# Kernel tuning notes

Measured on AMD Instinct MI355X. Metric: run time of the kernel, lower is better.

## Reference

```python
import jax, jax.numpy as jnp
import numpy as np

# Model dims (Gemma-class)
B, T, HID = 1, 3072, 2048
H, KH, D = 16, 8, 128          # q heads, kv heads, head_dim
WIN = 1024                     # sliding window
EPS = 1e-6
SEQ = 1536                     # two packed sequences of length 1536


def _rms(x, w):
    # torch nn.RMSNorm: x * rsqrt(mean(x^2) + eps) [* weight]
    var = jnp.mean(x * x, axis=-1, keepdims=True)
    y = x * jax.lax.rsqrt(var + EPS)
    return y if w is None else y * w


def _rotate_half(x):
    x1, x2 = jnp.split(x, 2, axis=-1)
    return jnp.concatenate([-x2, x1], axis=-1)


def _rope(x, cos, sin):
    # x: [B,T,h,D]; cos/sin: [B,T,rd] -> unsqueeze head dim (matches cos.unsqueeze(2))
    c = cos[:, :, None, :]
    s = sin[:, :, None, :]
    rd = cos.shape[-1]
    xr, xp = x[..., :rd], x[..., rd:]
    xr = xr * c + _rotate_half(xr) * s
    return jnp.concatenate([xr, xp], axis=-1)


def _build_mask(cu_seqlens):
    # causal & within sliding window & same packed sequence (matches _sliding_mask)
    idx = jnp.arange(T)
    seg = jnp.searchsorted(cu_seqlens, idx, side='right') - 1
    i = idx[:, None]
    j = idx[None, :]
    return (i >= j) & ((i - j) < WIN) & (seg[:, None] == seg[None, :])


def _attn_layer(x, wq, qn, k, v, wo, cos, sin, mask):
    # x: [B,T,HID]; k,v: [T,KH,D] (possibly shared from an earlier layer)
    q = _rope(_rms((x @ wq).reshape(B, T, H, D), qn), cos, sin).reshape(T, H, D)
    rep = H // k.shape[1]
    kk = jnp.repeat(k, rep, axis=1)   # GQA: repeat_interleave over head dim
    vv = jnp.repeat(v, rep, axis=1)
    s = jnp.einsum('qhd,khd->hqk', q, kk)          # scale = 1.0 (as in source)
    s = jnp.where(mask, s, jnp.asarray(-1e30, s.dtype))
    p = jax.nn.softmax(s, axis=-1)
    o = jnp.einsum('hqk,khd->qhd', p, vv).reshape(B, T, H * D)
    return o @ wo


def setup_inputs() -> dict:
    key = jax.random.key(0)
    ks = jax.random.split(key, 10)
    hidden_states = jax.random.normal(ks[0], (B, T, HID), jnp.float32)
    # RoPE tables with per-packed-sequence position resets
    pos = jnp.concatenate([jnp.arange(SEQ), jnp.arange(SEQ)]).astype(jnp.float32)
    inv = 1.0 / (10000.0 ** (jnp.arange(0, D, 2, dtype=jnp.float32) / D))
    fr = pos[:, None] * inv[None, :]
    emb = jnp.concatenate([fr, fr], axis=-1)     # [T, D]
    cos = jnp.cos(emb)[None]                     # [1, T, D]
    sin = jnp.sin(emb)[None]
    w = lambda k, sh: 0.02 * jax.random.normal(k, sh, jnp.float32)
    return {
        'hidden_states': hidden_states,
        'cos': cos, 'sin': sin,
        'wq0': w(ks[1], (HID, H * D)), 'wk0': w(ks[2], (HID, KH * D)),
        'wv0': w(ks[3], (HID, KH * D)), 'wo0': w(ks[4], (H * D, HID)),
        'qn0': 1.0 + 0.01 * jax.random.normal(ks[5], (D,), jnp.float32),
        'kn0': 1.0 + 0.01 * jax.random.normal(ks[6], (D,), jnp.float32),
        'wq1': w(ks[7], (HID, H * D)), 'wo1': w(ks[8], (H * D, HID)),
        'qn1': 1.0 + 0.01 * jax.random.normal(ks[9], (D,), jnp.float32),
        'cu_seqlens': jnp.array([0, SEQ, T], dtype=jnp.int32),
    }


def reference(hidden_states, cos, sin, wq0, wk0, wv0, wo0, qn0, kn0, wq1, wo1, qn1, cu_seqlens):
    mask = _build_mask(cu_seqlens)
    # Layer 0: source layer -> computes and stores K/V
    k = _rope(_rms((hidden_states @ wk0).reshape(B, T, KH, D), kn0), cos, sin).reshape(T, KH, D)
    v = _rms((hidden_states @ wv0).reshape(B, T, KH, D), None).reshape(T, KH, D)
    out0 = _attn_layer(hidden_states, wq0, qn0, k, v, wo0, cos, sin, mask)
    # Layer 1: KV-shared layer -> reuses layer 0's K/V (skips k/v projections)
    out1 = _attn_layer(out0, wq1, qn1, k, v, wo1, cos, sin, mask)
    return out1
```

## Files before the change

kernel.cpp:

```cpp
#include <hip/hip_runtime.h>
#include <hip/hip_bf16.h>

#define T_TOK 3072
#define HIDDEN 2048
#define NHQ 16
#define NHKV 8
#define DH 128
#define WINDOW 1024

typedef __attribute__((ext_vector_type(4))) float f32x4;
typedef __attribute__((ext_vector_type(8))) short bf16x8;
typedef __attribute__((ext_vector_type(8))) unsigned short ushort8;
typedef __attribute__((ext_vector_type(4))) unsigned short ushort4v;

__device__ __forceinline__ unsigned short f2bf(float f) {
  union { float fv; unsigned u; } v; v.fv = f;
  unsigned r = v.u + 0x7fffu + ((v.u >> 16) & 1u);
  return (unsigned short)(r >> 16);
}
__device__ __forceinline__ float bf2f(unsigned short h) {
  union { unsigned u; float f; } v; v.u = ((unsigned)h) << 16;
  return v.f;
}
__device__ __forceinline__ void split2(float f, unsigned short& hi, unsigned short& lo) {
  hi = f2bf(f);
  lo = f2bf(f - bf2f(hi));
}

__global__ __launch_bounds__(256) void cvt_split(const float* __restrict__ x,
                                                 unsigned short* __restrict__ yh,
                                                 unsigned short* __restrict__ yl, int n) {
  int i = (blockIdx.x * 256 + threadIdx.x) * 4;
  if (i >= n) return;
  f32x4 v = *(const f32x4*)(x + i);
  ushort4v oh, ol;
#pragma unroll
  for (int j = 0; j < 4; ++j) {
    unsigned short h, l;
    split2(v[j], h, l);
    oh[j] = h; ol[j] = l;
  }
  *(ushort4v*)(yh + i) = oh;
  *(ushort4v*)(yl + i) = ol;
}

__global__ __launch_bounds__(256) void transpose_w_split(const float* __restrict__ W,
                                                         unsigned short* __restrict__ Wth,
                                                         unsigned short* __restrict__ Wtl,
                                                         int K, int N) {
  __shared__ float tile[32][33];
  int bn = blockIdx.x * 32, bk = blockIdx.y * 32;
  int tx = threadIdx.x & 31, ty = threadIdx.x >> 5;
#pragma unroll
  for (int i = 0; i < 4; ++i)
    tile[ty + i * 8][tx] = W[(size_t)(bk + ty + i * 8) * N + bn + tx];
  __syncthreads();
#pragma unroll
  for (int i = 0; i < 4; ++i) {
    unsigned short h, l;
    split2(tile[tx][ty + i * 8], h, l);
    Wth[(size_t)(bn + ty + i * 8) * K + bk + tx] = h;
    if (Wtl) Wtl[(size_t)(bn + ty + i * 8) * K + bk + tx] = l;
  }
}

__global__ __launch_bounds__(256) void transpose_u16(const unsigned short* __restrict__ src,
                                                     unsigned short* __restrict__ dst,
                                                     int R, int C) {
  __shared__ unsigned short tile[32][33];
  int bc = blockIdx.x * 32, br = blockIdx.y * 32;
  int tx = threadIdx.x & 31, ty = threadIdx.x >> 5;
#pragma unroll
  for (int i = 0; i < 4; ++i)
    tile[ty + i * 8][tx] = src[(size_t)(br + ty + i * 8) * C + bc + tx];
  __syncthreads();
#pragma unroll
  for (int i = 0; i < 4; ++i)
    dst[(size_t)(bc + ty + i * 8) * R + br + tx] = tile[tx][ty + i * 8];
}

template <int OUT>
__global__ __launch_bounds__(256) void gemm3_64(const unsigned short* __restrict__ Ah,
                                                const unsigned short* __restrict__ Al,
                                                const unsigned short* __restrict__ Bh,
                                                const unsigned short* __restrict__ Bl,
                                                float* __restrict__ Cf,
                                                unsigned short* __restrict__ Ch,
                                                unsigned short* __restrict__ Cl,
                                                int M, int N, int K) {
  __shared__ unsigned short ah_lds[64 * 32];
  __shared__ unsigned short al_lds[64 * 32];
  __shared__ unsigned short bh_lds[128 * 32];
  __shared__ unsigned short bl_lds[128 * 32];
  const int tid = threadIdx.x, lane = tid & 63, wave = tid >> 6;
  const int wr = (wave >> 1) * 32, wc = (wave & 1) * 64;
  const int g = lane >> 4, r16 = lane & 15;
  int nwg = gridDim.x * gridDim.y;
  int id = blockIdx.y * gridDim.x + blockIdx.x;
  int nid = (id & 7) * (nwg >> 3) + (id >> 3);
  const int bm = nid % gridDim.x, bn = nid / gridDim.x;
  f32x4 acc[2][4];
#pragma unroll
  for (int i = 0; i < 2; ++i)
#pragma unroll
    for (int j = 0; j < 4; ++j) acc[i][j] = (f32x4){0.f, 0.f, 0.f, 0.f};

  const unsigned short* AhB = Ah + (size_t)bm * 64 * K;
  const unsigned short* AlB = Al + (size_t)bm * 64 * K;
  const unsigned short* BhB = Bh + (size_t)bn * 128 * K;
  const unsigned short* BlB = Bl + (size_t)bn * 128 * K;

  for (int kt = 0; kt < K; kt += 32) {
    __syncthreads();
    {
      size_t goff = (size_t)(wave * 16 + (lane >> 2)) * K + kt + (lane & 3) * 8;
      int loff = wave * 512;
      __builtin_amdgcn_global_load_lds(
          (const __attribute__((address_space(1))) unsigned int*)(AhB + goff),
          (__attribute__((address_space(3))) unsigned int*)(ah_lds + loff), 16, 0, 0);
      __builtin_amdgcn_global_load_lds(
          (const __attribute__((address_space(1))) unsigned int*)(AlB + goff),
          (__attribute__((address_space(3))) unsigned int*)(al_lds + loff), 16, 0, 0);
    }
#pragma unroll
    for (int c = 0; c < 2; ++c) {
      size_t goff = (size_t)(wave * 32 + c * 16 + (lane >> 2)) * K + kt + (lane & 3) * 8;
      int loff = (wave * 2 + c) * 512;
      __builtin_amdgcn_global_load_lds(
          (const __attribute__((address_space(1))) unsigned int*)(BhB + goff),
          (__attribute__((address_space(3))) unsigned int*)(bh_lds + loff), 16, 0, 0);
      __builtin_amdgcn_global_load_lds(
          (const __attribute__((address_space(1))) unsigned int*)(BlB + goff),
          (__attribute__((address_space(3))) unsigned int*)(bl_lds + loff), 16, 0, 0);
    }
    __syncthreads();
    bf16x8 ahf[2], alf[2], bhf[4], blf[4];
#pragma unroll
    for (int i = 0; i < 2; ++i) {
      ahf[i] = *(const bf16x8*)&ah_lds[(wr + i * 16 + r16) * 32 + g * 8];
      alf[i] = *(const bf16x8*)&al_lds[(wr + i * 16 + r16) * 32 + g * 8];
    }
#pragma unroll
    for (int j = 0; j < 4; ++j) {
      bhf[j] = *(const bf16x8*)&bh_lds[(wc + j * 16 + r16) * 32 + g * 8];
      blf[j] = *(const bf16x8*)&bl_lds[(wc + j * 16 + r16) * 32 + g * 8];
    }
#pragma unroll
    for (int i = 0; i < 2; ++i)
#pragma unroll
      for (int j = 0; j < 4; ++j) {
        acc[i][j] = __builtin_amdgcn_mfma_f32_16x16x32_bf16(ahf[i], bhf[j], acc[i][j], 0, 0, 0);
        acc[i][j] = __builtin_amdgcn_mfma_f32_16x16x32_bf16(ahf[i], blf[j], acc[i][j], 0, 0, 0);
        acc[i][j] = __builtin_amdgcn_mfma_f32_16x16x32_bf16(alf[i], bhf[j], acc[i][j], 0, 0, 0);
      }
  }

#pragma unroll
  for (int i = 0; i < 2; ++i) {
    int row = bm * 64 + wr + i * 16 + g * 4;
#pragma unroll
    for (int j = 0; j < 4; ++j) {
      int col = bn * 128 + wc + j * 16 + r16;
#pragma unroll
      for (int r = 0; r < 4; ++r) {
        if (OUT == 0) {
          Cf[(size_t)(row + r) * N + col] = acc[i][j][r];
        } else {
          unsigned short h, l;
          split2(acc[i][j][r], h, l);
          Ch[(size_t)(row + r) * N + col] = h;
          Cl[(size_t)(row + r) * N + col] = l;
        }
      }
    }
  }
}

__global__ __launch_bounds__(256) void gemm1_64(const unsigned short* __restrict__ Ah,
                                                const unsigned short* __restrict__ Bh,
                                                float* __restrict__ Cf,
                                                int M, int N, int K) {
  __shared__ unsigned short ah_lds[64 * 32];
  __shared__ unsigned short bh_lds[128 * 32];
  const int tid = threadIdx.x, lane = tid & 63, wave = tid >> 6;
  const int wr = (wave >> 1) * 32, wc = (wave & 1) * 64;
  const int g = lane >> 4, r16 = lane & 15;
  int nwg = gridDim.x * gridDim.y;
  int id = blockIdx.y * gridDim.x + blockIdx.x;
  int nid = (id & 7) * (nwg >> 3) + (id >> 3);
  const int bm = nid % gridDim.x, bn = nid / gridDim.x;
  f32x4 acc[2][4];
#pragma unroll
  for (int i = 0; i < 2; ++i)
#pragma unroll
    for (int j = 0; j < 4; ++j) acc[i][j] = (f32x4){0.f, 0.f, 0.f, 0.f};

  const unsigned short* AhB = Ah + (size_t)bm * 64 * K;
  const unsigned short* BhB = Bh + (size_t)bn * 128 * K;

  for (int kt = 0; kt < K; kt += 32) {
    __syncthreads();
    {
      size_t goff = (size_t)(wave * 16 + (lane >> 2)) * K + kt + (lane & 3) * 8;
      __builtin_amdgcn_global_load_lds(
          (const __attribute__((address_space(1))) unsigned int*)(AhB + goff),
          (__attribute__((address_space(3))) unsigned int*)(ah_lds + wave * 512), 16, 0, 0);
    }
#pragma unroll
    for (int c = 0; c < 2; ++c) {
      size_t goff = (size_t)(wave * 32 + c * 16 + (lane >> 2)) * K + kt + (lane & 3) * 8;
      __builtin_amdgcn_global_load_lds(
          (const __attribute__((address_space(1))) unsigned int*)(BhB + goff),
          (__attribute__((address_space(3))) unsigned int*)(bh_lds + (wave * 2 + c) * 512), 16, 0, 0);
    }
    __syncthreads();
    bf16x8 ahf[2], bhf[4];
#pragma unroll
    for (int i = 0; i < 2; ++i)
      ahf[i] = *(const bf16x8*)&ah_lds[(wr + i * 16 + r16) * 32 + g * 8];
#pragma unroll
    for (int j = 0; j < 4; ++j)
      bhf[j] = *(const bf16x8*)&bh_lds[(wc + j * 16 + r16) * 32 + g * 8];
#pragma unroll
    for (int i = 0; i < 2; ++i)
#pragma unroll
      for (int j = 0; j < 4; ++j)
        acc[i][j] = __builtin_amdgcn_mfma_f32_16x16x32_bf16(ahf[i], bhf[j], acc[i][j], 0, 0, 0);
  }

#pragma unroll
  for (int i = 0; i < 2; ++i) {
    int row = bm * 64 + wr + i * 16 + g * 4;
#pragma unroll
    for (int j = 0; j < 4; ++j) {
      int col = bn * 128 + wc + j * 16 + r16;
#pragma unroll
      for (int r = 0; r < 4; ++r)
        Cf[(size_t)(row + r) * N + col] = acc[i][j][r];
    }
  }
}

__global__ __launch_bounds__(256) void rms_rope_split(const float* __restrict__ X,
                                                      const float* __restrict__ w,
                                                      const float* __restrict__ cosp,
                                                      const float* __restrict__ sinp,
                                                      unsigned short* __restrict__ outh,
                                                      unsigned short* __restrict__ outl,
                                                      int NH, int doRope, int XS, int XO) {
  int row = blockIdx.x * 4 + (threadIdx.x >> 6);
  int lane = threadIdx.x & 63;
  int t = row / NH, hh_ = row % NH;
  const float* x = X + (size_t)t * XS + XO + (size_t)hh_ * DH;
  float x1 = x[lane], x2 = x[lane + 64];
  float ss = x1 * x1 + x2 * x2;
#pragma unroll
  for (int m = 1; m < 64; m <<= 1) ss += __shfl_xor(ss, m, 64);
  float inv = rsqrtf(ss * (1.0f / 128.0f) + 1e-6f);
  float y1 = x1 * inv, y2 = x2 * inv;
  if (w) { y1 *= w[lane]; y2 *= w[lane + 64]; }
  if (doRope) {
    float c1 = cosp[t * DH + lane], s1 = sinp[t * DH + lane];
    float c2 = cosp[t * DH + lane + 64], s2 = sinp[t * DH + lane + 64];
    float o1 = y1 * c1 - y2 * s1;
    float o2 = y2 * c2 + y1 * s2;
    y1 = o1; y2 = o2;
  }
  unsigned short h, l;
  split2(y1, h, l);
  outh[(size_t)row * DH + lane] = h;
  if (outl) outl[(size_t)row * DH + lane] = l;
  split2(y2, h, l);
  outh[(size_t)row * DH + lane + 64] = h;
  if (outl) outl[(size_t)row * DH + lane + 64] = l;
}

template <int WRITE_LO>
__global__ __launch_bounds__(256) void attn3(const unsigned short* __restrict__ Qh,
                                             const unsigned short* __restrict__ Ql,
                                             const unsigned short* __restrict__ Kh,
                                             const unsigned short* __restrict__ Kl,
                                             const unsigned short* __restrict__ Vth,
                                             unsigned short* __restrict__ Oh,
                                             unsigned short* __restrict__ Ol,
                                             const int* __restrict__ cu, int ncu) {
  __shared__ unsigned short kh_lds[32][136];
  __shared__ unsigned short kl_lds[32][136];
  __shared__ unsigned short vh_lds[144][40];
  __shared__ unsigned short ph_lds[4][16][44];

  int id = blockIdx.y * gridDim.x + blockIdx.x;
  int nid = (id & 7) * 96 + (id >> 3);
  const int qt = nid % 48, h = nid / 48;
  const int qbase = qt * 64;
  const int kvh = h >> 1;
  const int tid = threadIdx.x, lane = tid & 63, wave = tid >> 6;
  const int g = lane >> 4, r16 = lane & 15;

  for (int i = tid; i < 16 * 40; i += 256) {
    int rr = i / 40, cc = i % 40;
    vh_lds[128 + rr][cc] = (rr == 0) ? (unsigned short)0x3F80 : (unsigned short)0;
  }

  bf16x8 aqh[4], aql[4];
  {
    const size_t qoff = ((size_t)(qbase + wave * 16 + r16) * NHQ + h) * DH;
#pragma unroll
    for (int ks = 0; ks < 4; ++ks) {
      aqh[ks] = *(const bf16x8*)(Qh + qoff + ks * 32 + g * 8);
      aql[ks] = *(const bf16x8*)(Ql + qoff + ks * 32 + g * 8);
    }
  }

  int ssr[4];
#pragma unroll
  for (int r = 0; r < 4; ++r) {
    int q_r = qbase + wave * 16 + g * 4 + r;
    int s = 0;
    for (int i = 1; i < ncu; ++i) { int v = cu[i]; if (v <= q_r) s = v; }
    ssr[r] = s;
  }
  int ss_base = 0;
  for (int i = 1; i < ncu; ++i) { int v = cu[i]; if (v <= qbase) ss_base = v; }

  float m_r[4] = {-1e30f, -1e30f, -1e30f, -1e30f};
  f32x4 oacc[8];
#pragma unroll
  for (int db = 0; db < 8; ++db) oacc[db] = (f32x4){0.f, 0.f, 0.f, 0.f};
  f32x4 oaccL = (f32x4){0.f, 0.f, 0.f, 0.f};

  int lo = qbase - WINDOW + 1;
  if (lo < ss_base) lo = ss_base;
  if (lo < 0) lo = 0;
  int kt0 = lo & ~31;
  int ktend = qbase + 63;

  const int krow = tid >> 3, kcol = (tid & 7) * 16;
  const int vd = tid >> 1, vhalf = (tid & 1) * 16;
  const int qmin = qbase + wave * 16;

  ushort8 rkh0, rkh1, rkl0, rkl1, rvh0, rvh1;
  auto loadTile = [&](int kt) {
    size_t goff = ((size_t)(kt + krow) * NHKV + kvh) * DH + kcol;
    rkh0 = *(const ushort8*)(Kh + goff);
    rkh1 = *(const ushort8*)(Kh + goff + 8);
    rkl0 = *(const ushort8*)(Kl + goff);
    rkl1 = *(const ushort8*)(Kl + goff + 8);
    size_t voff = ((size_t)kvh * DH + vd) * T_TOK + kt + vhalf;
    rvh0 = *(const ushort8*)(Vth + voff);
    rvh1 = *(const ushort8*)(Vth + voff + 8);
  };
  auto writeTile = [&]() {
    *(ushort8*)&kh_lds[krow][kcol] = rkh0;
    *(ushort8*)&kh_lds[krow][kcol + 8] = rkh1;
    *(ushort8*)&kl_lds[krow][kcol] = rkl0;
    *(ushort8*)&kl_lds[krow][kcol + 8] = rkl1;
    *(ushort8*)&vh_lds[vd][vhalf] = rvh0;
    *(ushort8*)&vh_lds[vd][vhalf + 8] = rvh1;
  };

  loadTile(kt0);
  writeTile();
  __syncthreads();

  for (int kt = kt0; kt <= ktend; kt += 32) {
    const bool hasNext = (kt + 32 <= ktend);
    if (hasNext) loadTile(kt + 32);

    f32x4 s0 = (f32x4){0.f, 0.f, 0.f, 0.f}, s1 = (f32x4){0.f, 0.f, 0.f, 0.f};
#pragma unroll
    for (int ks = 0; ks < 4; ++ks) {
      bf16x8 bh0 = *(const bf16x8*)&kh_lds[r16][ks * 32 + g * 8];
      bf16x8 bh1 = *(const bf16x8*)&kh_lds[16 + r16][ks * 32 + g * 8];
      bf16x8 bl0 = *(const bf16x8*)&kl_lds[r16][ks * 32 + g * 8];
      bf16x8 bl1 = *(const bf16x8*)&kl_lds[16 + r16][ks * 32 + g * 8];
      s0 = __builtin_amdgcn_mfma_f32_16x16x32_bf16(aqh[ks], bh0, s0, 0, 0, 0);
      s0 = __builtin_amdgcn_mfma_f32_16x16x32_bf16(aqh[ks], bl0, s0, 0, 0, 0);
      s0 = __builtin_amdgcn_mfma_f32_16x16x32_bf16(aql[ks], bh0, s0, 0, 0, 0);
      s1 = __builtin_amdgcn_mfma_f32_16x16x32_bf16(aqh[ks], bh1, s1, 0, 0, 0);
      s1 = __builtin_amdgcn_mfma_f32_16x16x32_bf16(aqh[ks], bl1, s1, 0, 0, 0);
      s1 = __builtin_amdgcn_mfma_f32_16x16x32_bf16(aql[ks], bh1, s1, 0, 0, 0);
    }

    float sv0_[4], sv1_[4], mt_[4];
    bool ok0_[4], ok1_[4];
    bool interior = (kt + 31 <= qmin) && (kt >= qmin + 16 - WINDOW) &&
                    __all(kt >= ssr[3]);
    if (interior) {
#pragma unroll
      for (int r = 0; r < 4; ++r) {
        ok0_[r] = ok1_[r] = true;
        sv0_[r] = s0[r]; sv1_[r] = s1[r];
      }
    } else {
#pragma unroll
      for (int r = 0; r < 4; ++r) {
        int q_r = qmin + g * 4 + r;
        int k0 = kt + r16, k1 = k0 + 16;
        ok0_[r] = (k0 <= q_r) && (k0 > q_r - WINDOW) && (k0 >= ssr[r]);
        ok1_[r] = (k1 <= q_r) && (k1 > q_r - WINDOW) && (k1 >= ssr[r]);
        sv0_[r] = ok0_[r] ? s0[r] : -1e30f;
        sv1_[r] = ok1_[r] ? s1[r] : -1e30f;
      }
    }
#pragma unroll
    for (int r = 0; r < 4; ++r) {
      float mt = fmaxf(sv0_[r], sv1_[r]);
#pragma unroll
      for (int mm = 1; mm < 16; mm <<= 1) mt = fmaxf(mt, __shfl_xor(mt, mm, 64));
      mt_[r] = mt;
    }
    float grow = fmaxf(fmaxf(mt_[0] - m_r[0], mt_[1] - m_r[1]),
                       fmaxf(mt_[2] - m_r[2], mt_[3] - m_r[3]));
    if (!__all(grow <= 8.0f)) {
#pragma unroll
      for (int r = 0; r < 4; ++r) {
        float mnew = fmaxf(m_r[r], mt_[r]);
        float alpha = __expf(m_r[r] - mnew);
        m_r[r] = mnew;
#pragma unroll
        for (int db = 0; db < 8; ++db) oacc[db][r] *= alpha;
        oaccL[r] *= alpha;
      }
    }
#pragma unroll
    for (int r = 0; r < 4; ++r) {
      float p0v = ok0_[r] ? __expf(sv0_[r] - m_r[r]) : 0.f;
      float p1v = ok1_[r] ? __expf(sv1_[r] - m_r[r]) : 0.f;
      ph_lds[wave][g * 4 + r][r16] = f2bf(p0v);
      ph_lds[wave][g * 4 + r][16 + r16] = f2bf(p1v);
    }

    bf16x8 pah = *(const bf16x8*)&ph_lds[wave][r16][g * 8];
#pragma unroll
    for (int db = 0; db < 8; ++db) {
      bf16x8 vfh = *(const bf16x8*)&vh_lds[db * 16 + r16][g * 8];
      oacc[db] = __builtin_amdgcn_mfma_f32_16x16x32_bf16(pah, vfh, oacc[db], 0, 0, 0);
    }
    {
      bf16x8 vfo = *(const bf16x8*)&vh_lds[128 + r16][g * 8];
      oaccL = __builtin_amdgcn_mfma_f32_16x16x32_bf16(pah, vfo, oaccL, 0, 0, 0);
    }

    __syncthreads();
    if (hasNext) writeTile();
    __syncthreads();
  }

#pragma unroll
  for (int r = 0; r < 4; ++r) {
    int q_r = qbase + wave * 16 + g * 4 + r;
    float lsum = __shfl(oaccL[r], lane & 48, 64);
    float invl = 1.f / lsum;
#pragma unroll
    for (int db = 0; db < 8; ++db) {
      float ov = oacc[db][r] * invl;
      unsigned short hh, ll;
      split2(ov, hh, ll);
      Oh[(size_t)q_r * (NHQ * DH) + h * DH + db * 16 + r16] = hh;
      if (WRITE_LO) Ol[(size_t)q_r * (NHQ * DH) + h * DH + db * 16 + r16] = ll;
    }
  }
}

extern "C" void kernel_launch(void* const* d_in, const int* in_sizes, int n_in,
                              void* d_out, int out_size, void* d_ws, size_t ws_size,
                              hipStream_t stream) {
  const float* hidden = (const float*)d_in[0];
  const float* cosp   = (const float*)d_in[1];
  const float* sinp   = (const float*)d_in[2];
  const float* wq0    = (const float*)d_in[3];
  const float* wk0    = (const float*)d_in[4];
  const float* wv0    = (const float*)d_in[5];
  const float* wo0    = (const float*)d_in[6];
  const float* qn0    = (const float*)d_in[7];
  const float* kn0    = (const float*)d_in[8];
  const float* wq1    = (const float*)d_in[9];
  const float* wo1    = (const float*)d_in[10];
  const float* qn1    = (const float*)d_in[11];
  const int*   cu     = (const int*)d_in[12];
  int ncu = in_sizes[12];

  char* p = (char*)d_ws;
  auto alloc = [&](size_t bytes) { char* r = p; p += (bytes + 255) & ~255ull; return r; };
  float*          c32  = (float*)alloc((size_t)T_TOK * HIDDEN * 4);
  unsigned short* xh   = (unsigned short*)alloc((size_t)T_TOK * HIDDEN * 2);
  unsigned short* xl   = (unsigned short*)alloc((size_t)T_TOK * HIDDEN * 2);
  unsigned short* wth  = (unsigned short*)alloc((size_t)HIDDEN * HIDDEN * 2);
  unsigned short* wtl  = (unsigned short*)alloc((size_t)HIDDEN * HIDDEN * 2);
  unsigned short* qh   = (unsigned short*)alloc((size_t)T_TOK * NHQ * DH * 2);
  unsigned short* ql   = (unsigned short*)alloc((size_t)T_TOK * NHQ * DH * 2);
  unsigned short* kh   = (unsigned short*)alloc((size_t)T_TOK * NHKV * DH * 2);
  unsigned short* kl   = (unsigned short*)alloc((size_t)T_TOK * NHKV * DH * 2);
  unsigned short* vh   = (unsigned short*)alloc((size_t)T_TOK * NHKV * DH * 2);
  unsigned short* vth  = (unsigned short*)alloc((size_t)T_TOK * NHKV * DH * 2);
  unsigned short* x1h  = (unsigned short*)alloc((size_t)T_TOK * HIDDEN * 2);
  unsigned short* x1l  = (unsigned short*)alloc((size_t)T_TOK * HIDDEN * 2);
  (void)ws_size; (void)n_in; (void)out_size;

  const int nX = T_TOK * HIDDEN;
  const int KVN = NHKV * DH;

  cvt_split<<<nX / 1024, 256, 0, stream>>>(hidden, xh, xl, nX);

  transpose_w_split<<<dim3(HIDDEN / 32, HIDDEN / 32), 256, 0, stream>>>(wq0, wth, wtl, HIDDEN, HIDDEN);
  gemm3_64<0><<<dim3(T_TOK / 64, HIDDEN / 128), 256, 0, stream>>>(xh, xl, wth, wtl, c32, nullptr, nullptr, T_TOK, HIDDEN, HIDDEN);
  rms_rope_split<<<T_TOK * NHQ / 4, 256, 0, stream>>>(c32, qn0, cosp, sinp, qh, ql, NHQ, 1, HIDDEN, 0);

  transpose_w_split<<<dim3(KVN / 32, HIDDEN / 32), 256, 0, stream>>>(wk0, wth, wtl, HIDDEN, KVN);
  transpose_w_split<<<dim3(KVN / 32, HIDDEN / 32), 256, 0, stream>>>(
      wv0, wth + (size_t)KVN * HIDDEN, wtl + (size_t)KVN * HIDDEN, HIDDEN, KVN);
  gemm3_64<0><<<dim3(T_TOK / 64, (2 * KVN) / 128), 256, 0, stream>>>(xh, xl, wth, wtl, c32, nullptr, nullptr, T_TOK, 2 * KVN, HIDDEN);
  rms_rope_split<<<T_TOK * NHKV / 4, 256, 0, stream>>>(c32, kn0, cosp, sinp, kh, kl, NHKV, 1, 2 * KVN, 0);
  rms_rope_split<<<T_TOK * NHKV / 4, 256, 0, stream>>>(c32, nullptr, cosp, sinp, vh, nullptr, NHKV, 0, 2 * KVN, KVN);

  transpose_u16<<<dim3(KVN / 32, T_TOK / 32), 256, 0, stream>>>(vh, vth, T_TOK, KVN);

  attn3<1><<<dim3(T_TOK / 64, NHQ), 256, 0, stream>>>(qh, ql, kh, kl, vth, xh, xl, cu, ncu);

  transpose_w_split<<<dim3(HIDDEN / 32, HIDDEN / 32), 256, 0, stream>>>(wo0, wth, wtl, HIDDEN, HIDDEN);
  gemm3_64<2><<<dim3(T_TOK / 64, HIDDEN / 128), 256, 0, stream>>>(xh, xl, wth, wtl, nullptr, x1h, x1l, T_TOK, HIDDEN, HIDDEN);

  transpose_w_split<<<dim3(HIDDEN / 32, HIDDEN / 32), 256, 0, stream>>>(wq1, wth, wtl, HIDDEN, HIDDEN);
  gemm3_64<0><<<dim3(T_TOK / 64, HIDDEN / 128), 256, 0, stream>>>(x1h, x1l, wth, wtl, c32, nullptr, nullptr, T_TOK, HIDDEN, HIDDEN);
  rms_rope_split<<<T_TOK * NHQ / 4, 256, 0, stream>>>(c32, qn1, cosp, sinp, qh, ql, NHQ, 1, HIDDEN, 0);

  attn3<0><<<dim3(T_TOK / 64, NHQ), 256, 0, stream>>>(qh, ql, kh, kl, vth, xh, nullptr, cu, ncu);

  transpose_w_split<<<dim3(HIDDEN / 32, HIDDEN / 32), 256, 0, stream>>>(wo1, wth, nullptr, HIDDEN, HIDDEN);
  gemm1_64<<<dim3(T_TOK / 64, HIDDEN / 128), 256, 0, stream>>>(xh, wth, (float*)d_out, T_TOK, HIDDEN, HIDDEN);
}
```

Measured before the change: 753.7 us.

## Fuse QKV projection into one 128x128 GEMM, retile GEMMs, swizzle attention K LDS

Adds a 128x128-tile split-bf16 GEMM that computes the Q, K and V projections of layer 0 in one launch when the workspace is large enough, writing Q and KV into separate fp32 buffers. The remaining projection GEMMs move from 64-row to 96-row tiles, which gives more reuse per block and fewer blocks. The attention kernel's K tile in LDS gets an XOR-like rotation swizzle to reduce bank conflicts on the MFMA fragment reads. A fallback path keeps separate GEMMs for small workspaces. The trade-offs are larger per-block register and LDS use, fewer waves per CU, and buffer aliasing of V onto the Q scratch buffer.

```diff
diff --git a/kernel.cpp b/kernel.cpp
--- a/kernel.cpp
+++ b/kernel.cpp
@@ -79,8 +79,90 @@
     dst[(size_t)(bc + ty + i * 8) * R + br + tx] = tile[tx][ty + i * 8];
 }
 
+__global__ __launch_bounds__(256) void gemm3_128(const unsigned short* __restrict__ Ah,
+                                                 const unsigned short* __restrict__ Al,
+                                                 const unsigned short* __restrict__ Bh,
+                                                 const unsigned short* __restrict__ Bl,
+                                                 float* __restrict__ Cq,
+                                                 float* __restrict__ Ckv,
+                                                 int strd, int M, int N, int K) {
+  __shared__ unsigned short ah_lds[128 * 32];
+  __shared__ unsigned short al_lds[128 * 32];
+  __shared__ unsigned short bh_lds[128 * 32];
+  __shared__ unsigned short bl_lds[128 * 32];
+  const int tid = threadIdx.x, lane = tid & 63, wave = tid >> 6;
+  const int wr = (wave >> 1) * 64, wc = (wave & 1) * 64;
+  const int g = lane >> 4, r16 = lane & 15;
+  int nwg = gridDim.x * gridDim.y;
+  int id = blockIdx.y * gridDim.x + blockIdx.x;
+  int nid = (id & 7) * (nwg >> 3) + (id >> 3);
+  const int bm = nid % gridDim.x, bn = nid / gridDim.x;
+  f32x4 acc[4][4];
+#pragma unroll
+  for (int i = 0; i < 4; ++i)
+#pragma unroll
+    for (int j = 0; j < 4; ++j) acc[i][j] = (f32x4){0.f, 0.f, 0.f, 0.f};
+
+  const unsigned short* AhB = Ah + (size_t)bm * 128 * K;
+  const unsigned short* AlB = Al + (size_t)bm * 128 * K;
+  const unsigned short* BhB = Bh + (size_t)bn * 128 * K;
+  const unsigned short* BlB = Bl + (size_t)bn * 128 * K;
+
+  for (int kt = 0; kt < K; kt += 32) {
+    __syncthreads();
+#pragma unroll
+    for (int c = 0; c < 2; ++c) {
+      size_t goff = (size_t)(wave * 32 + c * 16 + (lane >> 2)) * K + kt + (lane & 3) * 8;
+      int loff = (wave * 2 + c) * 512;
+      __builtin_amdgcn_global_load_lds(
+          (const __attribute__((address_space(1))) unsigned int*)(AhB + goff),
+          (__attribute__((address_space(3))) unsigned int*)(ah_lds + loff), 16, 0, 0);
+      __builtin_amdgcn_global_load_lds(
+          (const __attribute__((address_space(1))) unsigned int*)(AlB + goff),
+          (__attribute__((address_space(3))) unsigned int*)(al_lds + loff), 16, 0, 0);
+      __builtin_amdgcn_global_load_lds(
+          (const __attribute__((address_space(1))) unsigned int*)(BhB + goff),
+          (__attribute__((address_space(3))) unsigned int*)(bh_lds + loff), 16, 0, 0);
+      __builtin_amdgcn_global_load_lds(
+          (const __attribute__((address_space(1))) unsigned int*)(BlB + goff),
+          (__attribute__((address_space(3))) unsigned int*)(bl_lds + loff), 16, 0, 0);
+    }
+    __syncthreads();
+    bf16x8 ahf[4], alf[4], bhf[4], blf[4];
+#pragma unroll
+    for (int i = 0; i < 4; ++i) {
+      ahf[i] = *(const bf16x8*)&ah_lds[(wr + i * 16 + r16) * 32 + g * 8];
+      alf[i] = *(const bf16x8*)&al_lds[(wr + i * 16 + r16) * 32 + g * 8];
+      bhf[i] = *(const bf16x8*)&bh_lds[(wc + i * 16 + r16) * 32 + g * 8];
+      blf[i] = *(const bf16x8*)&bl_lds[(wc + i * 16 + r16) * 32 + g * 8];
+    }
+#pragma unroll
+    for (int i = 0; i < 4; ++i)
+#pragma unroll
+      for (int j = 0; j < 4; ++j) {
+        acc[i][j] = __builtin_amdgcn_mfma_f32_16x16x32_bf16(ahf[i], bhf[j], acc[i][j], 0, 0, 0);
+        acc[i][j] = __builtin_amdgcn_mfma_f32_16x16x32_bf16(ahf[i], blf[j], acc[i][j], 0, 0, 0);
+        acc[i][j] = __builtin_amdgcn_mfma_f32_16x16x32_bf16(alf[i], bhf[j], acc[i][j], 0, 0, 0);
+      }
+  }
+
+#pragma unroll
+  for (int i = 0; i < 4; ++i) {
+    int row = bm * 128 + wr + i * 16 + g * 4;
+#pragma unroll
+    for (int j = 0; j < 4; ++j) {
+      int colg = bn * 128 + wc + j * 16 + r16;
+      float* Cb; int cc;
+      if (colg < 2048) { Cb = Cq; cc = colg; } else { Cb = Ckv; cc = colg - 2048; }
+#pragma unroll
+      for (int r = 0; r < 4; ++r)
+        Cb[(size_t)(row + r) * strd + cc] = acc[i][j][r];
+    }
+  }
+}
+
 template <int OUT>
-__global__ __launch_bounds__(256) void gemm3_64(const unsigned short* __restrict__ Ah,
+__global__ __launch_bounds__(256) void gemm3_96(const unsigned short* __restrict__ Ah,
                                                 const unsigned short* __restrict__ Al,
                                                 const unsigned short* __restrict__ Bh,
                                                 const unsigned short* __restrict__ Bl,
@@ -88,39 +170,49 @@
                                                 unsigned short* __restrict__ Ch,
                                                 unsigned short* __restrict__ Cl,
                                                 int M, int N, int K) {
-  __shared__ unsigned short ah_lds[64 * 32];
-  __shared__ unsigned short al_lds[64 * 32];
+  __shared__ unsigned short ah_lds[96 * 32];
+  __shared__ unsigned short al_lds[96 * 32];
   __shared__ unsigned short bh_lds[128 * 32];
   __shared__ unsigned short bl_lds[128 * 32];
   const int tid = threadIdx.x, lane = tid & 63, wave = tid >> 6;
-  const int wr = (wave >> 1) * 32, wc = (wave & 1) * 64;
+  const int wr = (wave >> 1) * 48, wc = (wave & 1) * 64;
   const int g = lane >> 4, r16 = lane & 15;
   int nwg = gridDim.x * gridDim.y;
   int id = blockIdx.y * gridDim.x + blockIdx.x;
   int nid = (id & 7) * (nwg >> 3) + (id >> 3);
   const int bm = nid % gridDim.x, bn = nid / gridDim.x;
-  f32x4 acc[2][4];
-#pragma unroll
-  for (int i = 0; i < 2; ++i)
+  f32x4 acc[3][4];
+#pragma unroll
+  for (int i = 0; i < 3; ++i)
 #pragma unroll
     for (int j = 0; j < 4; ++j) acc[i][j] = (f32x4){0.f, 0.f, 0.f, 0.f};
 
-  const unsigned short* AhB = Ah + (size_t)bm * 64 * K;
-  const unsigned short* AlB = Al + (size_t)bm * 64 * K;
+  const unsigned short* AhB = Ah + (size_t)bm * 96 * K;
+  const unsigned short* AlB = Al + (size_t)bm * 96 * K;
   const unsigned short* BhB = Bh + (size_t)bn * 128 * K;
   const unsigned short* BlB = Bl + (size_t)bn * 128 * K;
 
   for (int kt = 0; kt < K; kt += 32) {
     __syncthreads();
     {
-      size_t goff = (size_t)(wave * 16 + (lane >> 2)) * K + kt + (lane & 3) * 8;
-      int loff = wave * 512;
+      int c = wave;
+      size_t goff = (size_t)(c * 16 + (lane >> 2)) * K + kt + (lane & 3) * 8;
       __builtin_amdgcn_global_load_lds(
           (const __attribute__((address_space(1))) unsigned int*)(AhB + goff),
-          (__attribute__((address_space(3))) unsigned int*)(ah_lds + loff), 16, 0, 0);
+          (__attribute__((address_space(3))) unsigned int*)(ah_lds + c * 512), 16, 0, 0);
       __builtin_amdgcn_global_load_lds(
           (const __attribute__((address_space(1))) unsigned int*)(AlB + goff),
-          (__attribute__((address_space(3))) unsigned int*)(al_lds + loff), 16, 0, 0);
+          (__attribute__((address_space(3))) unsigned int*)(al_lds + c * 512), 16, 0, 0);
+      if (wave < 2) {
+        int c2 = 4 + wave;
+        size_t goff2 = (size_t)(c2 * 16 + (lane >> 2)) * K + kt + (lane & 3) * 8;
+        __builtin_amdgcn_global_load_lds(
+            (const __attribute__((address_space(1))) unsigned int*)(AhB + goff2),
+            (__attribute__((address_space(3))) unsigned int*)(ah_lds + c2 * 512), 16, 0, 0);
+        __builtin_amdgcn_global_load_lds(
+            (const __attribute__((address_space(1))) unsigned int*)(AlB + goff2),
+            (__attribute__((address_space(3))) unsigned int*)(al_lds + c2 * 512), 16, 0, 0);
+      }
     }
 #pragma unroll
     for (int c = 0; c < 2; ++c) {
@@ -134,9 +226,9 @@
           (__attribute__((address_space(3))) unsigned int*)(bl_lds + loff), 16, 0, 0);
     }
     __syncthreads();
-    bf16x8 ahf[2], alf[2], bhf[4], blf[4];
-#pragma unroll
-    for (int i = 0; i < 2; ++i) {
+    bf16x8 ahf[3], alf[3], bhf[4], blf[4];
+#pragma unroll
+    for (int i = 0; i < 3; ++i) {
       ahf[i] = *(const bf16x8*)&ah_lds[(wr + i * 16 + r16) * 32 + g * 8];
       alf[i] = *(const bf16x8*)&al_lds[(wr + i * 16 + r16) * 32 + g * 8];
     }
@@ -146,7 +238,7 @@
       blf[j] = *(const bf16x8*)&bl_lds[(wc + j * 16 + r16) * 32 + g * 8];
     }
 #pragma unroll
-    for (int i = 0; i < 2; ++i)
+    for (int i = 0; i < 3; ++i)
 #pragma unroll
       for (int j = 0; j < 4; ++j) {
         acc[i][j] = __builtin_amdgcn_mfma_f32_16x16x32_bf16(ahf[i], bhf[j], acc[i][j], 0, 0, 0);
@@ -156,8 +248,8 @@
   }
 
 #pragma unroll
-  for (int i = 0; i < 2; ++i) {
-    int row = bm * 64 + wr + i * 16 + g * 4;
+  for (int i = 0; i < 3; ++i) {
+    int row = bm * 96 + wr + i * 16 + g * 4;
 #pragma unroll
     for (int j = 0; j < 4; ++j) {
       int col = bn * 128 + wc + j * 16 + r16;
@@ -176,35 +268,43 @@
   }
 }
 
-__global__ __launch_bounds__(256) void gemm1_64(const unsigned short* __restrict__ Ah,
+__global__ __launch_bounds__(256) void gemm1_96(const unsigned short* __restrict__ Ah,
                                                 const unsigned short* __restrict__ Bh,
                                                 float* __restrict__ Cf,
                                                 int M, int N, int K) {
-  __shared__ unsigned short ah_lds[64 * 32];
+  __shared__ unsigned short ah_lds[96 * 32];
   __shared__ unsigned short bh_lds[128 * 32];
   const int tid = threadIdx.x, lane = tid & 63, wave = tid >> 6;
-  const int wr = (wave >> 1) * 32, wc = (wave & 1) * 64;
+  const int wr = (wave >> 1) * 48, wc = (wave & 1) * 64;
   const int g = lane >> 4, r16 = lane & 15;
   int nwg = gridDim.x * gridDim.y;
   int id = blockIdx.y * gridDim.x + blockIdx.x;
   int nid = (id & 7) * (nwg >> 3) + (id >> 3);
   const int bm = nid % gridDim.x, bn = nid / gridDim.x;
-  f32x4 acc[2][4];
-#pragma unroll
-  for (int i = 0; i < 2; ++i)
+  f32x4 acc[3][4];
+#pragma unroll
+  for (int i = 0; i < 3; ++i)
 #pragma unroll
     for (int j = 0; j < 4; ++j) acc[i][j] = (f32x4){0.f, 0.f, 0.f, 0.f};
 
-  const unsigned short* AhB = Ah + (size_t)bm * 64 * K;
+  const unsigned short* AhB = Ah + (size_t)bm * 96 * K;
   const unsigned short* BhB = Bh + (size_t)bn * 128 * K;
 
   for (int kt = 0; kt < K; kt += 32) {
     __syncthreads();
     {
-      size_t goff = (size_t)(wave * 16 + (lane >> 2)) * K + kt + (lane & 3) * 8;
+      int c = wave;
+      size_t goff = (size_t)(c * 16 + (lane >> 2)) * K + kt + (lane & 3) * 8;
       __builtin_amdgcn_global_load_lds(
           (const __attribute__((address_space(1))) unsigned int*)(AhB + goff),
-          (__attribute__((address_space(3))) unsigned int*)(ah_lds + wave * 512), 16, 0, 0);
+          (__attribute__((address_space(3))) unsigned int*)(ah_lds + c * 512), 16, 0, 0);
+      if (wave < 2) {
+        int c2 = 4 + wave;
+        size_t goff2 = (size_t)(c2 * 16 + (lane >> 2)) * K + kt + (lane & 3) * 8;
+        __builtin_amdgcn_global_load_lds(
+            (const __attribute__((address_space(1))) unsigned int*)(AhB + goff2),
+            (__attribute__((address_space(3))) unsigned int*)(ah_lds + c2 * 512), 16, 0, 0);
+      }
     }
 #pragma unroll
     for (int c = 0; c < 2; ++c) {
@@ -214,23 +314,23 @@
           (__attribute__((address_space(3))) unsigned int*)(bh_lds + (wave * 2 + c) * 512), 16, 0, 0);
     }
     __syncthreads();
-    bf16x8 ahf[2], bhf[4];
-#pragma unroll
-    for (int i = 0; i < 2; ++i)
+    bf16x8 ahf[3], bhf[4];
+#pragma unroll
+    for (int i = 0; i < 3; ++i)
       ahf[i] = *(const bf16x8*)&ah_lds[(wr + i * 16 + r16) * 32 + g * 8];
 #pragma unroll
     for (int j = 0; j < 4; ++j)
       bhf[j] = *(const bf16x8*)&bh_lds[(wc + j * 16 + r16) * 32 + g * 8];
 #pragma unroll
-    for (int i = 0; i < 2; ++i)
+    for (int i = 0; i < 3; ++i)
 #pragma unroll
       for (int j = 0; j < 4; ++j)
         acc[i][j] = __builtin_amdgcn_mfma_f32_16x16x32_bf16(ahf[i], bhf[j], acc[i][j], 0, 0, 0);
   }
 
 #pragma unroll
-  for (int i = 0; i < 2; ++i) {
-    int row = bm * 64 + wr + i * 16 + g * 4;
+  for (int i = 0; i < 3; ++i) {
+    int row = bm * 96 + wr + i * 16 + g * 4;
 #pragma unroll
     for (int j = 0; j < 4; ++j) {
       int col = bn * 128 + wc + j * 16 + r16;
@@ -335,26 +435,30 @@
   int kt0 = lo & ~31;
   int ktend = qbase + 63;
 
-  const int krow = tid >> 3, kcol = (tid & 7) * 16;
+  const int krow = tid >> 3, kc = tid & 7;
   const int vd = tid >> 1, vhalf = (tid & 1) * 16;
   const int qmin = qbase + wave * 16;
+  const int sw0 = ((kc + (krow & 15)) & 15) * 16;
+  const int sw1 = ((kc + 8 + (krow & 15)) & 15) * 16;
 
   ushort8 rkh0, rkh1, rkl0, rkl1, rvh0, rvh1;
   auto loadTile = [&](int kt) {
-    size_t goff = ((size_t)(kt + krow) * NHKV + kvh) * DH + kcol;
+    size_t goff = ((size_t)(kt + krow) * NHKV + kvh) * DH + kc * 8;
     rkh0 = *(const ushort8*)(Kh + goff);
-    rkh1 = *(const ushort8*)(Kh + goff + 8);
+    rkh1 = *(const ushort8*)(Kh + goff + 64);
     rkl0 = *(const ushort8*)(Kl + goff);
-    rkl1 = *(const ushort8*)(Kl + goff + 8);
+    rkl1 = *(const ushort8*)(Kl + goff + 64);
     size_t voff = ((size_t)kvh * DH + vd) * T_TOK + kt + vhalf;
     rvh0 = *(const ushort8*)(Vth + voff);
     rvh1 = *(const ushort8*)(Vth + voff + 8);
   };
   auto writeTile = [&]() {
-    *(ushort8*)&kh_lds[krow][kcol] = rkh0;
-    *(ushort8*)&kh_lds[krow][kcol + 8] = rkh1;
-    *(ushort8*)&kl_lds[krow][kcol] = rkl0;
-    *(ushort8*)&kl_lds[krow][kcol + 8] = rkl1;
+    char* kbh = (char*)&kh_lds[krow][0];
+    char* kbl = (char*)&kl_lds[krow][0];
+    *(ushort8*)(kbh + sw0) = rkh0;
+    *(ushort8*)(kbh + sw1) = rkh1;
+    *(ushort8*)(kbl + sw0) = rkl0;
+    *(ushort8*)(kbl + sw1) = rkl1;
     *(ushort8*)&vh_lds[vd][vhalf] = rvh0;
     *(ushort8*)&vh_lds[vd][vhalf + 8] = rvh1;
   };
@@ -368,18 +472,25 @@
     if (hasNext) loadTile(kt + 32);
 
     f32x4 s0 = (f32x4){0.f, 0.f, 0.f, 0.f}, s1 = (f32x4){0.f, 0.f, 0.f, 0.f};
-#pragma unroll
-    for (int ks = 0; ks < 4; ++ks) {
-      bf16x8 bh0 = *(const bf16x8*)&kh_lds[r16][ks * 32 + g * 8];
-      bf16x8 bh1 = *(const bf16x8*)&kh_lds[16 + r16][ks * 32 + g * 8];
-      bf16x8 bl0 = *(const bf16x8*)&kl_lds[r16][ks * 32 + g * 8];
-      bf16x8 bl1 = *(const bf16x8*)&kl_lds[16 + r16][ks * 32 + g * 8];
-      s0 = __builtin_amdgcn_mfma_f32_16x16x32_bf16(aqh[ks], bh0, s0, 0, 0, 0);
-      s0 = __builtin_amdgcn_mfma_f32_16x16x32_bf16(aqh[ks], bl0, s0, 0, 0, 0);
-      s0 = __builtin_amdgcn_mfma_f32_16x16x32_bf16(aql[ks], bh0, s0, 0, 0, 0);
-      s1 = __builtin_amdgcn_mfma_f32_16x16x32_bf16(aqh[ks], bh1, s1, 0, 0, 0);
-      s1 = __builtin_amdgcn_mfma_f32_16x16x32_bf16(aqh[ks], bl1, s1, 0, 0, 0);
-      s1 = __builtin_amdgcn_mfma_f32_16x16x32_bf16(aql[ks], bh1, s1, 0, 0, 0);
+    {
+      const char* kb0h = (const char*)&kh_lds[r16][0];
+      const char* kb1h = (const char*)&kh_lds[16 + r16][0];
+      const char* kb0l = (const char*)&kl_lds[r16][0];
+      const char* kb1l = (const char*)&kl_lds[16 + r16][0];
+#pragma unroll
+      for (int ks = 0; ks < 4; ++ks) {
+        int sl = ((ks * 4 + g + r16) & 15) * 16;
+        bf16x8 bh0 = *(const bf16x8*)(kb0h + sl);
+        bf16x8 bh1 = *(const bf16x8*)(kb1h + sl);
+        bf16x8 bl0 = *(const bf16x8*)(kb0l + sl);
+        bf16x8 bl1 = *(const bf16x8*)(kb1l + sl);
+        s0 = __builtin_amdgcn_mfma_f32_16x16x32_bf16(aqh[ks], bh0, s0, 0, 0, 0);
+        s0 = __builtin_amdgcn_mfma_f32_16x16x32_bf16(aqh[ks], bl0, s0, 0, 0, 0);
+        s0 = __builtin_amdgcn_mfma_f32_16x16x32_bf16(aql[ks], bh0, s0, 0, 0, 0);
+        s1 = __builtin_amdgcn_mfma_f32_16x16x32_bf16(aqh[ks], bh1, s1, 0, 0, 0);
+        s1 = __builtin_amdgcn_mfma_f32_16x16x32_bf16(aqh[ks], bl1, s1, 0, 0, 0);
+        s1 = __builtin_amdgcn_mfma_f32_16x16x32_bf16(aql[ks], bh1, s1, 0, 0, 0);
+      }
     }
 
     float sv0_[4], sv1_[4], mt_[4];
@@ -480,53 +591,113 @@
   const float* qn1    = (const float*)d_in[11];
   const int*   cu     = (const int*)d_in[12];
   int ncu = in_sizes[12];
+  (void)n_in; (void)out_size;
+
+  const int nX = T_TOK * HIDDEN;
+  const int KVN = NHKV * DH;
 
   char* p = (char*)d_ws;
   auto alloc = [&](size_t bytes) { char* r = p; p += (bytes + 255) & ~255ull; return r; };
-  float*          c32  = (float*)alloc((size_t)T_TOK * HIDDEN * 4);
-  unsigned short* xh   = (unsigned short*)alloc((size_t)T_TOK * HIDDEN * 2);
-  unsigned short* xl   = (unsigned short*)alloc((size_t)T_TOK * HIDDEN * 2);
-  unsigned short* wth  = (unsigned short*)alloc((size_t)HIDDEN * HIDDEN * 2);
-  unsigned short* wtl  = (unsigned short*)alloc((size_t)HIDDEN * HIDDEN * 2);
-  unsigned short* qh   = (unsigned short*)alloc((size_t)T_TOK * NHQ * DH * 2);
-  unsigned short* ql   = (unsigned short*)alloc((size_t)T_TOK * NHQ * DH * 2);
-  unsigned short* kh   = (unsigned short*)alloc((size_t)T_TOK * NHKV * DH * 2);
-  unsigned short* kl   = (unsigned short*)alloc((size_t)T_TOK * NHKV * DH * 2);
-  unsigned short* vh   = (unsigned short*)alloc((size_t)T_TOK * NHKV * DH * 2);
-  unsigned short* vth  = (unsigned short*)alloc((size_t)T_TOK * NHKV * DH * 2);
-  unsigned short* x1h  = (unsigned short*)alloc((size_t)T_TOK * HIDDEN * 2);
-  unsigned short* x1l  = (unsigned short*)alloc((size_t)T_TOK * HIDDEN * 2);
-  (void)ws_size; (void)n_in; (void)out_size;
-
-  const int nX = T_TOK * HIDDEN;
-  const int KVN = NHKV * DH;
-
-  cvt_split<<<nX / 1024, 256, 0, stream>>>(hidden, xh, xl, nX);
-
-  transpose_w_split<<<dim3(HIDDEN / 32, HIDDEN / 32), 256, 0, stream>>>(wq0, wth, wtl, HIDDEN, HIDDEN);
-  gemm3_64<0><<<dim3(T_TOK / 64, HIDDEN / 128), 256, 0, stream>>>(xh, xl, wth, wtl, c32, nullptr, nullptr, T_TOK, HIDDEN, HIDDEN);
-  rms_rope_split<<<T_TOK * NHQ / 4, 256, 0, stream>>>(c32, qn0, cosp, sinp, qh, ql, NHQ, 1, HIDDEN, 0);
-
-  transpose_w_split<<<dim3(KVN / 32, HIDDEN / 32), 256, 0, stream>>>(wk0, wth, wtl, HIDDEN, KVN);
-  transpose_w_split<<<dim3(KVN / 32, HIDDEN / 32), 256, 0, stream>>>(
-      wv0, wth + (size_t)KVN * HIDDEN, wtl + (size_t)KVN * HIDDEN, HIDDEN, KVN);
-  gemm3_64<0><<<dim3(T_TOK / 64, (2 * KVN) / 128), 256, 0, stream>>>(xh, xl, wth, wtl, c32, nullptr, nullptr, T_TOK, 2 * KVN, HIDDEN);
-  rms_rope_split<<<T_TOK * NHKV / 4, 256, 0, stream>>>(c32, kn0, cosp, sinp, kh, kl, NHKV, 1, 2 * KVN, 0);
-  rms_rope_split<<<T_TOK * NHKV / 4, 256, 0, stream>>>(c32, nullptr, cosp, sinp, vh, nullptr, NHKV, 0, 2 * KVN, KVN);
-
-  transpose_u16<<<dim3(KVN / 32, T_TOK / 32), 256, 0, stream>>>(vh, vth, T_TOK, KVN);
-
-  attn3<1><<<dim3(T_TOK / 64, NHQ), 256, 0, stream>>>(qh, ql, kh, kl, vth, xh, xl, cu, ncu);
-
-  transpose_w_split<<<dim3(HIDDEN / 32, HIDDEN / 32), 256, 0, stream>>>(wo0, wth, wtl, HIDDEN, HIDDEN);
-  gemm3_64<2><<<dim3(T_TOK / 64, HIDDEN / 128), 256, 0, stream>>>(xh, xl, wth, wtl, nullptr, x1h, x1l, T_TOK, HIDDEN, HIDDEN);
-
-  transpose_w_split<<<dim3(HIDDEN / 32, HIDDEN / 32), 256, 0, stream>>>(wq1, wth, wtl, HIDDEN, HIDDEN);
-  gemm3_64<0><<<dim3(T_TOK / 64, HIDDEN / 128), 256, 0, stream>>>(x1h, x1l, wth, wtl, c32, nullptr, nullptr, T_TOK, HIDDEN, HIDDEN);
-  rms_rope_split<<<T_TOK * NHQ / 4, 256, 0, stream>>>(c32, qn1, cosp, sinp, qh, ql, NHQ, 1, HIDDEN, 0);
-
-  attn3<0><<<dim3(T_TOK / 64, NHQ), 256, 0, stream>>>(qh, ql, kh, kl, vth, xh, nullptr, cu, ncu);
-
-  transpose_w_split<<<dim3(HIDDEN / 32, HIDDEN / 32), 256, 0, stream>>>(wo1, wth, nullptr, HIDDEN, HIDDEN);
-  gemm1_64<<<dim3(T_TOK / 64, HIDDEN / 128), 256, 0, stream>>>(xh, wth, (float*)d_out, T_TOK, HIDDEN, HIDDEN);
-}
+
+  const size_t NEED_FUSED = 173ull * 1024 * 1024;
+  bool fusedOK = (ws_size >= NEED_FUSED);
+
+  if (fusedOK) {
+    float*          c32q  = (float*)alloc((size_t)T_TOK * HIDDEN * 4);
+    float*          c32kv = (float*)alloc((size_t)T_TOK * HIDDEN * 4);
+    unsigned short* xh    = (unsigned short*)alloc((size_t)T_TOK * HIDDEN * 2);
+    unsigned short* xl    = (unsigned short*)alloc((size_t)T_TOK * HIDDEN * 2);
+    unsigned short* wth   = (unsigned short*)alloc((size_t)2 * HIDDEN * HIDDEN * 2);
+    unsigned short* wtl   = (unsigned short*)alloc((size_t)2 * HIDDEN * HIDDEN * 2);
+    unsigned short* qh    = (unsigned short*)alloc((size_t)T_TOK * NHQ * DH * 2);
+    unsigned short* ql    = (unsigned short*)alloc((size_t)T_TOK * NHQ * DH * 2);
+    unsigned short* kh    = (unsigned short*)alloc((size_t)T_TOK * KVN * 2);
+    unsigned short* kl    = (unsigned short*)alloc((size_t)T_TOK * KVN * 2);
+    unsigned short* x1h   = (unsigned short*)alloc((size_t)T_TOK * HIDDEN * 2);
+    unsigned short* x1l   = (unsigned short*)alloc((size_t)T_TOK * HIDDEN * 2);
+    unsigned short* vh    = (unsigned short*)c32q;
+    unsigned short* vth   = vh + (size_t)T_TOK * KVN;
+
+    cvt_split<<<nX / 1024, 256, 0, stream>>>(hidden, xh, xl, nX);
+
+    transpose_w_split<<<dim3(HIDDEN / 32, HIDDEN / 32), 256, 0, stream>>>(wq0, wth, wtl, HIDDEN, HIDDEN);
+    transpose_w_split<<<dim3(KVN / 32, HIDDEN / 32), 256, 0, stream>>>(
+        wk0, wth + (size_t)HIDDEN * HIDDEN, wtl + (size_t)HIDDEN * HIDDEN, HIDDEN, KVN);
+    transpose_w_split<<<dim3(KVN / 32, HIDDEN / 32), 256, 0, stream>>>(
+        wv0, wth + (size_t)(HIDDEN + KVN) * HIDDEN, wtl + (size_t)(HIDDEN + KVN) * HIDDEN, HIDDEN, KVN);
+
+    gemm3_128<<<dim3(T_TOK / 128, 4096 / 128), 256, 0, stream>>>(
+        xh, xl, wth, wtl, c32q, c32kv, HIDDEN, T_TOK, 4096, HIDDEN);
+
+    rms_rope_split<<<T_TOK * NHQ / 4, 256, 0, stream>>>(c32q, qn0, cosp, sinp, qh, ql, NHQ, 1, HIDDEN, 0);
+    rms_rope_split<<<T_TOK * NHKV / 4, 256, 0, stream>>>(c32kv, kn0, cosp, sinp, kh, kl, NHKV, 1, HIDDEN, 0);
+    rms_rope_split<<<T_TOK * NHKV / 4, 256, 0, stream>>>(c32kv, nullptr, cosp, sinp, vh, nullptr, NHKV, 0, HIDDEN, KVN);
+
+    transpose_u16<<<dim3(KVN / 32, T_TOK / 32), 256, 0, stream>>>(vh, vth, T_TOK, KVN);
+
+    attn3<1><<<dim3(T_TOK / 64, NHQ), 256, 0, stream>>>(qh, ql, kh, kl, vth, xh, xl, cu, ncu);
+
+    transpose_w_split<<<dim3(HIDDEN / 32, HIDDEN / 32), 256, 0, stream>>>(wo0, wth, wtl, HIDDEN, HIDDEN);
+    gemm3_96<2><<<dim3(T_TOK / 96, HIDDEN / 128), 256, 0, stream>>>(
+        xh, xl, wth, wtl, nullptr, x1h, x1l, T_TOK, HIDDEN, HIDDEN);
+
+    transpose_w_split<<<dim3(HIDDEN / 32, HIDDEN / 32), 256, 0, stream>>>(wq1, wth, wtl, HIDDEN, HIDDEN);
+    gemm3_96<0><<<dim3(T_TOK / 96, HIDDEN / 128), 256, 0, stream>>>(
+        x1h, x1l, wth, wtl, c32kv, nullptr, nullptr, T_TOK, HIDDEN, HIDDEN);
+    rms_rope_split<<<T_TOK * NHQ / 4, 256, 0, stream>>>(c32kv, qn1, cosp, sinp, qh, ql, NHQ, 1, HIDDEN, 0);
+
+    attn3<0><<<dim3(T_TOK / 64, NHQ), 256, 0, stream>>>(qh, ql, kh, kl, vth, xh, nullptr, cu, ncu);
+
+    transpose_w_split<<<dim3(HIDDEN / 32, HIDDEN / 32), 256, 0, stream>>>(wo1, wth, nullptr, HIDDEN, HIDDEN);
+    gemm1_96<<<dim3(T_TOK / 96, HIDDEN / 128), 256, 0, stream>>>(xh, wth, (float*)d_out, T_TOK, HIDDEN, HIDDEN);
+  } else {
+    float*          c32  = (float*)alloc((size_t)T_TOK * HIDDEN * 4);
+    unsigned short* xh   = (unsigned short*)alloc((size_t)T_TOK * HIDDEN * 2);
+    unsigned short* xl   = (unsigned short*)alloc((size_t)T_TOK * HIDDEN * 2);
+    unsigned short* wth  = (unsigned short*)alloc((size_t)HIDDEN * HIDDEN * 2);
+    unsigned short* wtl  = (unsigned short*)alloc((size_t)HIDDEN * HIDDEN * 2);
+    unsigned short* qh   = (unsigned short*)alloc((size_t)T_TOK * NHQ * DH * 2);
+    unsigned short* ql   = (unsigned short*)alloc((size_t)T_TOK * NHQ * DH * 2);
+    unsigned short* kh   = (unsigned short*)alloc((size_t)T_TOK * KVN * 2);
+    unsigned short* kl   = (unsigned short*)alloc((size_t)T_TOK * KVN * 2);
+    unsigned short* vh   = (unsigned short*)alloc((size_t)T_TOK * KVN * 2);
+    unsigned short* vth  = (unsigned short*)alloc((size_t)T_TOK * KVN * 2);
+    unsigned short* x1h  = (unsigned short*)alloc((size_t)T_TOK * HIDDEN * 2);
+    unsigned short* x1l  = (unsigned short*)alloc((size_t)T_TOK * HIDDEN * 2);
+
+    cvt_split<<<nX / 1024, 256, 0, stream>>>(hidden, xh, xl, nX);
+
+    transpose_w_split<<<dim3(HIDDEN / 32, HIDDEN / 32), 256, 0, stream>>>(wq0, wth, wtl, HIDDEN, HIDDEN);
+    gemm3_128<<<dim3(T_TOK / 128, HIDDEN / 128), 256, 0, stream>>>(
+        xh, xl, wth, wtl, c32, c32, HIDDEN, T_TOK, HIDDEN, HIDDEN);
+    rms_rope_split<<<T_TOK * NHQ / 4, 256, 0, stream>>>(c32, qn0, cosp, sinp, qh, ql, NHQ, 1, HIDDEN, 0);
+
+    transpose_w_split<<<dim3(KVN / 32, HIDDEN / 32), 256, 0, stream>>>(wk0, wth, wtl, HIDDEN, KVN);
+    gemm3_128<<<dim3(T_TOK / 128, KVN / 128), 256, 0, stream>>>(
+        xh, xl, wth, wtl, c32, c32, KVN, T_TOK, KVN, HIDDEN);
+    rms_rope_split<<<T_TOK * NHKV / 4, 256, 0, stream>>>(c32, kn0, cosp, sinp, kh, kl, NHKV, 1, KVN, 0);
+
+    transpose_w_split<<<dim3(KVN / 32, HIDDEN / 32), 256, 0, stream>>>(wv0, wth, wtl, HIDDEN, KVN);
+    gemm3_128<<<dim3(T_TOK / 128, KVN / 128), 256, 0, stream>>>(
+        xh, xl, wth, wtl, c32, c32, KVN, T_TOK, KVN, HIDDEN);
+    rms_rope_split<<<T_TOK * NHKV / 4, 256, 0, stream>>>(c32, nullptr, cosp, sinp, vh, nullptr, NHKV, 0, KVN, 0);
+
+    transpose_u16<<<dim3(KVN / 32, T_TOK / 32), 256, 0, stream>>>(vh, vth, T_TOK, KVN);
+
+    attn3<1><<<dim3(T_TOK / 64, NHQ), 256, 0, stream>>>(qh, ql, kh, kl, vth, xh, xl, cu, ncu);
+
+    transpose_w_split<<<dim3(HIDDEN / 32, HIDDEN / 32), 256, 0, stream>>>(wo0, wth, wtl, HIDDEN, HIDDEN);
+    gemm3_96<2><<<dim3(T_TOK / 96, HIDDEN / 128), 256, 0, stream>>>(
+        xh, xl, wth, wtl, nullptr, x1h, x1l, T_TOK, HIDDEN, HIDDEN);
+
+    transpose_w_split<<<dim3(HIDDEN / 32, HIDDEN / 32), 256, 0, stream>>>(wq1, wth, wtl, HIDDEN, HIDDEN);
+    gemm3_96<0><<<dim3(T_TOK / 96, HIDDEN / 128), 256, 0, stream>>>(
+        x1h, x1l, wth, wtl, c32, nullptr, nullptr, T_TOK, HIDDEN, HIDDEN);
+    rms_rope_split<<<T_TOK * NHQ / 4, 256, 0, stream>>>(c32, qn1, cosp, sinp, qh, ql, NHQ, 1, HIDDEN, 0);
+
+    attn3<0><<<dim3(T_TOK / 64, NHQ), 256, 0, stream>>>(qh, ql, kh, kl, vth, xh, nullptr, cu, ncu);
+
+    transpose_w_split<<<dim3(HIDDEN / 32, HIDDEN / 32), 256, 0, stream>>>(wo1, wth, nullptr, HIDDEN, HIDDEN);
+    gemm1_96<<<dim3(T_TOK / 96, HIDDEN / 128), 256, 0, stream>>>(xh, wth, (float*)d_out, T_TOK, HIDDEN, HIDDEN);
+  }
+}
```

Result: faster. 676.2 us (-10.3%).
